# Performance work log

Hardware: AMD Instinct MI355X
Metric: run time of the kernel (lower is better)

## Reference

```python
import jax, jax.numpy as jnp
import numpy as np

B, S, H, A, E = 64, 1024, 1024, 512, 512


def setup_inputs() -> dict:
    key = jax.random.key(0)
    ks = jax.random.split(key, 13)
    sc = 0.02
    return {
        "inputs": jax.random.normal(ks[0], (B, E), jnp.float32),
        "states": jax.random.normal(ks[1], (B, H), jnp.float32),
        "encoded": jax.random.normal(ks[2], (B, S, H), jnp.float32),
        "W_enc": jax.random.normal(ks[3], (H, A), jnp.float32) * sc,
        "b_enc": jax.random.normal(ks[4], (A,), jnp.float32) * sc,
        "W_dec": jax.random.normal(ks[5], (H, A), jnp.float32) * sc,
        "b_dec": jax.random.normal(ks[6], (A,), jnp.float32) * sc,
        "w_out": jax.random.normal(ks[7], (A,), jnp.float32) * sc,
        "b_out": jax.random.normal(ks[8], (1,), jnp.float32) * sc,
        "W_ih": jax.random.normal(ks[9], (E + H, 3 * H), jnp.float32) * sc,
        "b_ih": jax.random.normal(ks[10], (3 * H,), jnp.float32) * sc,
        "W_hh": jax.random.normal(ks[11], (H, 3 * H), jnp.float32) * sc,
        "b_hh": jax.random.normal(ks[12], (3 * H,), jnp.float32) * sc,
    }


def reference(inputs, states, encoded, W_enc, b_enc, W_dec, b_dec, w_out, b_out,
              W_ih, b_ih, W_hh, b_hh):
    # setup_memory: project encoder states once  [B,S,H] @ [H,A] -> [B,S,A]
    enc_proj = jnp.einsum('bsh,ha->bsa', encoded, W_enc) + b_enc
    # Bahdanau additive attention
    dec_proj = states @ W_dec + b_dec                       # [B,A]
    scores = jnp.einsum('bsa,a->bs', jnp.tanh(enc_proj + dec_proj[:, None, :]), w_out) + b_out[0]
    weights = jax.nn.softmax(scores, axis=1)                # [B,S]
    attention = jnp.einsum('bs,bsh->bh', weights, encoded)  # [B,H]
    x = jnp.concatenate([inputs, attention], axis=-1)       # [B,E+H]
    # GRUCell (PyTorch gate order r, z, n)
    gi = x @ W_ih + b_ih                                    # [B,3H]
    gh = states @ W_hh + b_hh                               # [B,3H]
    i_r, i_z, i_n = jnp.split(gi, 3, axis=-1)
    h_r, h_z, h_n = jnp.split(gh, 3, axis=-1)
    r = jax.nn.sigmoid(i_r + h_r)
    z = jax.nn.sigmoid(i_z + h_z)
    n = jnp.tanh(i_n + r * h_n)
    h_new = (1.0 - z) * n + z * states
    return h_new
```

## Files before the change

kernel.cpp:

```cpp
#include <hip/hip_runtime.h>
#include <hip/hip_bf16.h>


typedef __attribute__((ext_vector_type(8))) __bf16 bf16x8;
typedef __attribute__((ext_vector_type(4))) __bf16 bf16x4;
typedef __attribute__((ext_vector_type(4))) float f32x4;

__device__ __forceinline__ float fast_tanh(float x) {
  float xa = fminf(fmaxf(x, -15.f), 15.f);
  float e = __expf(2.f * xa);
  return (e - 1.f) / (e + 1.f);
}

#define GLOAD16(G, L)                                                              \
  __builtin_amdgcn_global_load_lds(                                                \
      (const __attribute__((address_space(1))) unsigned int*)(const void*)(G),     \
      (__attribute__((address_space(3))) unsigned int*)(void*)(L), 16, 0, 0)

__global__ __launch_bounds__(256) void conv_kernel(const float* __restrict__ in,
                                                   __bf16* __restrict__ out, long n16) {
  long stride = (long)gridDim.x * 256;
  for (long i = (long)blockIdx.x * 256 + threadIdx.x; i < n16; i += stride) {
    const f32x4* p = (const f32x4*)(in + i * 16);
    f32x4 v0 = p[0], v1 = p[1], v2 = p[2], v3 = p[3];
    bf16x8 o0, o1;
#pragma unroll
    for (int j = 0; j < 4; ++j) {
      o0[j] = (__bf16)v0[j]; o0[4 + j] = (__bf16)v1[j];
      o1[j] = (__bf16)v2[j]; o1[4 + j] = (__bf16)v3[j];
    }
    *(bf16x8*)(out + i * 16) = o0;
    *(bf16x8*)(out + i * 16 + 8) = o1;
  }
}

__global__ __launch_bounds__(256) void wenc_t_kernel(const float* __restrict__ W,
                                                     __bf16* __restrict__ Wt) {
  __shared__ float tile[32][33];
  int k0 = blockIdx.x * 32, a0 = blockIdx.y * 32;
  int tid = threadIdx.x;
  int r = tid >> 3, c4 = (tid & 7) * 4;
  f32x4 v = *(const f32x4*)(W + (long)(k0 + r) * 512 + a0 + c4);
  tile[r][c4 + 0] = v.x; tile[r][c4 + 1] = v.y;
  tile[r][c4 + 2] = v.z; tile[r][c4 + 3] = v.w;
  __syncthreads();
  int a = tid >> 3, k4 = (tid & 7) * 4;
  bf16x4 o = { (__bf16)tile[k4 + 0][a], (__bf16)tile[k4 + 1][a],
               (__bf16)tile[k4 + 2][a], (__bf16)tile[k4 + 3][a] };
  *(bf16x4*)(Wt + (long)(a0 + a) * 1024 + k0 + k4) = o;
}

__global__ __launch_bounds__(256) void dec_proj_kernel(
    const float* __restrict__ states, const float* __restrict__ W_dec,
    const float* __restrict__ b_enc, const float* __restrict__ b_dec,
    float* __restrict__ addv) {
  int b = blockIdx.x, tid = threadIdx.x;
  int a = blockIdx.y * 256 + tid;
  __shared__ float sl[1024];
  for (int i = tid; i < 1024; i += 256) sl[i] = states[b * 1024 + i];
  __syncthreads();
  float c0 = 0.f, c1 = 0.f, c2 = 0.f, c3 = 0.f;
#pragma unroll 4
  for (int i = 0; i < 256; ++i) {
    c0 += sl[i]         * W_dec[(i)        * 512 + a];
    c1 += sl[i + 256]   * W_dec[(i + 256)  * 512 + a];
    c2 += sl[i + 512]   * W_dec[(i + 512)  * 512 + a];
    c3 += sl[i + 768]   * W_dec[(i + 768)  * 512 + a];
  }
  addv[b * 512 + a] = c0 + c1 + c2 + c3 + b_enc[a] + b_dec[a];
}

__global__ __launch_bounds__(512, 2) void enc_score_kernel(
    const __bf16* __restrict__ encB,
    const __bf16* __restrict__ Wt,
    const float* __restrict__ addv,
    const float* __restrict__ w_out,
    float* __restrict__ psc)
{
  __shared__ __attribute__((aligned(16))) char smem[102400];
  float* red = (float*)(smem + 98304);

  const int d = blockIdx.x;
  const int xcd = d & 7;
  const int slot = d >> 3;
  const int bn = slot & 1;
  const int bm = ((slot >> 1) << 3) | xcd;

  const int tid = threadIdx.x;
  const int lane = tid & 63;
  const int wid = tid >> 6;
  const int wr = wid >> 2;
  const int wc = wid & 3;
  const int lr = lane & 15;
  const int lkb = lane >> 4;

  const long row0 = (long)bm * 256;
  const int col0 = bn * 256;

  const int sk8 = (tid & 3) ^ ((tid >> 3) & 3);
  const __bf16* gA = encB + (row0 + (tid >> 2)) * 1024 + sk8 * 8;
  const __bf16* gB = Wt + (long)(col0 + (tid >> 2)) * 1024 + sk8 * 8;
  const int ldsW = wid * 1024;

  const int foff = (lkb ^ ((lr >> 1) & 3)) << 4;
  const int aRowB = (wr * 128 + lr) * 64;
  const int bColB = (wc * 64 + lr) * 64;

  f32x4 acc[8][4];
#pragma unroll
  for (int m = 0; m < 8; ++m)
#pragma unroll
    for (int n = 0; n < 4; ++n) acc[m][n] = (f32x4){0.f, 0.f, 0.f, 0.f};

#define STAGE(SBUF, KT) do {                                                       \
    const __bf16* _a = gA + (KT) * 32;                                             \
    const __bf16* _b = gB + (KT) * 32;                                             \
    GLOAD16(_a,          smem + (SBUF) * 16384 + ldsW);                            \
    GLOAD16(_a + 131072, smem + (SBUF) * 16384 + 8192 + ldsW);                     \
    GLOAD16(_b,          smem + 49152 + (SBUF) * 16384 + ldsW);                    \
    GLOAD16(_b + 131072, smem + 49152 + (SBUF) * 16384 + 8192 + ldsW);             \
    __builtin_amdgcn_sched_barrier(0);                                             \
  } while (0)

#define COMPUTE(CBUF) do {                                                         \
    const char* _Ab = smem + (CBUF) * 16384;                                       \
    const char* _Bb = smem + 49152 + (CBUF) * 16384;                               \
    bf16x8 _af[8], _bv[4];                                                         \
    _Pragma("unroll") for (int _m = 0; _m < 8; ++_m)                               \
      _af[_m] = *(const bf16x8*)(_Ab + aRowB + _m * 1024 + foff);                  \
    _Pragma("unroll") for (int _n = 0; _n < 4; ++_n)                               \
      _bv[_n] = *(const bf16x8*)(_Bb + bColB + _n * 1024 + foff);                  \
    __builtin_amdgcn_s_setprio(1);                                                 \
    _Pragma("unroll") for (int _m = 0; _m < 8; ++_m)                               \
      _Pragma("unroll") for (int _n = 0; _n < 4; ++_n)                             \
        acc[_m][_n] =                                                              \
            __builtin_amdgcn_mfma_f32_16x16x32_bf16(_af[_m], _bv[_n], acc[_m][_n], 0, 0, 0); \
    __builtin_amdgcn_s_setprio(0);                                                 \
  } while (0)

#define ITER(KT, CBUF, SBUF) do {                                                  \
    asm volatile("s_waitcnt vmcnt(4)" ::: "memory");                               \
    __builtin_amdgcn_sched_barrier(0);                                             \
    __builtin_amdgcn_s_barrier();                                                  \
    __builtin_amdgcn_sched_barrier(0);                                             \
    COMPUTE(CBUF);                                                                 \
    asm volatile("s_waitcnt lgkmcnt(0)" ::: "memory");                             \
    __builtin_amdgcn_sched_barrier(0);                                             \
    __builtin_amdgcn_s_barrier();                                                  \
    __builtin_amdgcn_sched_barrier(0);                                             \
    STAGE(SBUF, (KT) + 2);                                                         \
  } while (0)

  STAGE(0, 0);
  STAGE(1, 1);

  for (int k3 = 0; k3 < 30; k3 += 3) {
    ITER(k3 + 0, 0, 2);
    ITER(k3 + 1, 1, 0);
    ITER(k3 + 2, 2, 1);
  }
  asm volatile("s_waitcnt vmcnt(4)" ::: "memory");
  __builtin_amdgcn_sched_barrier(0);
  __builtin_amdgcn_s_barrier();
  __builtin_amdgcn_sched_barrier(0);
  COMPUTE(0);
  asm volatile("s_waitcnt vmcnt(0)" ::: "memory");
  __builtin_amdgcn_sched_barrier(0);
  __builtin_amdgcn_s_barrier();
  __builtin_amdgcn_sched_barrier(0);
  COMPUTE(1);

#undef STAGE
#undef COMPUTE
#undef ITER

  const int b = bm >> 2;
  const float* addvb = addv + b * 512;
  float rowsum[8][4];
#pragma unroll
  for (int m = 0; m < 8; ++m)
#pragma unroll
    for (int reg = 0; reg < 4; ++reg) rowsum[m][reg] = 0.f;

#pragma unroll
  for (int m = 0; m < 8; ++m) {
#pragma unroll
    for (int n = 0; n < 4; ++n) {
      int col = col0 + wc * 64 + n * 16 + lr;
      float av = addvb[col];
      float wo = w_out[col];
#pragma unroll
      for (int reg = 0; reg < 4; ++reg)
        rowsum[m][reg] += fast_tanh(acc[m][n][reg] + av) * wo;
    }
  }
#pragma unroll
  for (int m = 0; m < 8; ++m)
#pragma unroll
    for (int reg = 0; reg < 4; ++reg) {
      float v = rowsum[m][reg];
      v += __shfl_xor(v, 1, 64);
      v += __shfl_xor(v, 2, 64);
      v += __shfl_xor(v, 4, 64);
      v += __shfl_xor(v, 8, 64);
      rowsum[m][reg] = v;
    }
  __syncthreads();
  if (lr == 0) {
#pragma unroll
    for (int m = 0; m < 8; ++m)
#pragma unroll
      for (int reg = 0; reg < 4; ++reg)
        red[(wr * 128 + m * 16 + lkb * 4 + reg) * 4 + wc] = rowsum[m][reg];
  }
  __syncthreads();
  if (tid < 256)
    psc[(long)bn * 65536 + row0 + tid] =
        red[tid * 4] + red[tid * 4 + 1] + red[tid * 4 + 2] + red[tid * 4 + 3];
}

__global__ __launch_bounds__(256) void softmax_kernel(const float* __restrict__ psc,
                                                      float* __restrict__ wts) {
  int b = blockIdx.x, tid = threadIdx.x;
  __shared__ float sred[8];
  float sc[4];
  float mx = -1e30f;
#pragma unroll
  for (int i = 0; i < 4; ++i) {
    long r = (long)b * 1024 + tid + i * 256;
    sc[i] = psc[r] + psc[65536 + r];
    mx = fmaxf(mx, sc[i]);
  }
  for (int off = 1; off < 64; off <<= 1) mx = fmaxf(mx, __shfl_xor(mx, off, 64));
  if ((tid & 63) == 0) sred[tid >> 6] = mx;
  __syncthreads();
  mx = fmaxf(fmaxf(sred[0], sred[1]), fmaxf(sred[2], sred[3]));
  float e[4], sum = 0.f;
#pragma unroll
  for (int i = 0; i < 4; ++i) {
    e[i] = __expf(sc[i] - mx);
    sum += e[i];
  }
  for (int off = 1; off < 64; off <<= 1) sum += __shfl_xor(sum, off, 64);
  if ((tid & 63) == 0) sred[4 + (tid >> 6)] = sum;
  __syncthreads();
  sum = sred[4] + sred[5] + sred[6] + sred[7];
  float inv = 1.f / sum;
#pragma unroll
  for (int i = 0; i < 4; ++i) wts[(long)b * 1024 + tid + i * 256] = e[i] * inv;
}

__global__ __launch_bounds__(128) void att_part_bf16_kernel(const __bf16* __restrict__ encB,
                                                            const float* __restrict__ wts,
                                                            float* __restrict__ attp) {
  int chunk = blockIdx.x;
  int b = blockIdx.y;
  int tid = threadIdx.x;
  const __bf16* base = encB + ((long)b * 1024 + chunk * 64) * 1024 + tid * 8;
  const float* w = wts + b * 1024 + chunk * 64;
  float a0[8], a1[8];
#pragma unroll
  for (int j = 0; j < 8; ++j) { a0[j] = 0.f; a1[j] = 0.f; }
#pragma unroll 4
  for (int s = 0; s < 64; s += 2) {
    bf16x8 v0 = *(const bf16x8*)(base + (long)s * 1024);
    bf16x8 v1 = *(const bf16x8*)(base + (long)(s + 1) * 1024);
    float w0 = w[s], w1 = w[s + 1];
#pragma unroll
    for (int j = 0; j < 8; ++j) {
      a0[j] += (float)v0[j] * w0;
      a1[j] += (float)v1[j] * w1;
    }
  }
  float* o = attp + ((long)(b * 16 + chunk)) * 1024 + tid * 8;
#pragma unroll
  for (int j = 0; j < 8; ++j) o[j] = a0[j] + a1[j];
}

__global__ __launch_bounds__(256) void xcat_kernel(const float* __restrict__ inputs,
                                                   const float* __restrict__ attp,
                                                   float* __restrict__ xcat) {
  int b = blockIdx.y;
  int k = blockIdx.x * 256 + threadIdx.x;
  float v;
  if (k < 512) {
    v = inputs[b * 512 + k];
  } else {
    int h = k - 512;
    v = 0.f;
#pragma unroll
    for (int c = 0; c < 16; ++c) v += attp[((long)(b * 16 + c)) * 1024 + h];
  }
  xcat[(long)b * 1536 + k] = v;
}

__global__ __launch_bounds__(512) void gru_gemv_kernel(
    const float* __restrict__ xcat, const float* __restrict__ states,
    const float* __restrict__ W_ih, const float* __restrict__ b_ih,
    const float* __restrict__ W_hh, const float* __restrict__ b_hh,
    float* __restrict__ gi, float* __restrict__ gh) {
  __shared__ float sx[12288];
  const int dd = blockIdx.x;
  const int xcd = dd & 7;
  const int n = dd >> 3;
  const int cgrp = xcd + 8 * (n >> 3);
  const int bg = n & 7;
  const int tid = threadIdx.x;
  const int lcol = tid & 255;
  const int bsel = (tid >> 8) * 4;

  if (cgrp < 12) {
    const int col = cgrp * 256 + lcol;
    const float* xb = xcat + (long)bg * 8 * 1536;
    for (int i = tid; i < 3072; i += 512) ((f32x4*)sx)[i] = ((const f32x4*)xb)[i];
    __syncthreads();
    float a0 = b_ih[col], a1 = a0, a2 = a0, a3 = a0;
    const float* x0 = sx + (bsel + 0) * 1536;
    const float* x1 = sx + (bsel + 1) * 1536;
    const float* x2 = sx + (bsel + 2) * 1536;
    const float* x3 = sx + (bsel + 3) * 1536;
    for (int k = 0; k < 1536; k += 4) {
      f32x4 v0 = *(const f32x4*)(x0 + k);
      f32x4 v1 = *(const f32x4*)(x1 + k);
      f32x4 v2 = *(const f32x4*)(x2 + k);
      f32x4 v3 = *(const f32x4*)(x3 + k);
#pragma unroll
      for (int j = 0; j < 4; ++j) {
        float w = W_ih[(long)(k + j) * 3072 + col];
        a0 += v0[j] * w; a1 += v1[j] * w; a2 += v2[j] * w; a3 += v3[j] * w;
      }
    }
    long o = (long)(bg * 8 + bsel) * 3072 + col;
    gi[o] = a0; gi[o + 3072] = a1; gi[o + 6144] = a2; gi[o + 9216] = a3;
  } else {
    const int col = (cgrp - 12) * 256 + lcol;
    const float* sb = states + (long)bg * 8 * 1024;
    for (int i = tid; i < 2048; i += 512) ((f32x4*)sx)[i] = ((const f32x4*)sb)[i];
    __syncthreads();
    float a0 = b_hh[col], a1 = a0, a2 = a0, a3 = a0;
    const float* x0 = sx + (bsel + 0) * 1024;
    const float* x1 = sx + (bsel + 1) * 1024;
    const float* x2 = sx + (bsel + 2) * 1024;
    const float* x3 = sx + (bsel + 3) * 1024;
    for (int k = 0; k < 1024; k += 4) {
      f32x4 v0 = *(const f32x4*)(x0 + k);
      f32x4 v1 = *(const f32x4*)(x1 + k);
      f32x4 v2 = *(const f32x4*)(x2 + k);
      f32x4 v3 = *(const f32x4*)(x3 + k);
#pragma unroll
      for (int j = 0; j < 4; ++j) {
        float w = W_hh[(long)(k + j) * 3072 + col];
        a0 += v0[j] * w; a1 += v1[j] * w; a2 += v2[j] * w; a3 += v3[j] * w;
      }
    }
    long o = (long)(bg * 8 + bsel) * 3072 + col;
    gh[o] = a0; gh[o + 3072] = a1; gh[o + 6144] = a2; gh[o + 9216] = a3;
  }
}

__global__ __launch_bounds__(256) void gate_kernel(const float* __restrict__ gi,
                                                   const float* __restrict__ gh,
                                                   const float* __restrict__ states,
                                                   float* __restrict__ out) {
  int b = blockIdx.y;
  int j = blockIdx.x * 256 + threadIdx.x;
  long o = (long)b * 3072;
  float ir = gi[o + j], hr = gh[o + j];
  float iz = gi[o + 1024 + j], hz = gh[o + 1024 + j];
  float in_ = gi[o + 2048 + j], hn = gh[o + 2048 + j];
  float r = 1.f / (1.f + __expf(-(ir + hr)));
  float z = 1.f / (1.f + __expf(-(iz + hz)));
  float n = fast_tanh(in_ + r * hn);
  out[(long)b * 1024 + j] = (1.f - z) * n + z * states[(long)b * 1024 + j];
}

extern "C" void kernel_launch(void* const* d_in, const int* in_sizes, int n_in,
                              void* d_out, int out_size, void* d_ws, size_t ws_size,
                              hipStream_t stream) {
  const float* inputs  = (const float*)d_in[0];
  const float* states  = (const float*)d_in[1];
  const float* encoded = (const float*)d_in[2];
  const float* W_enc   = (const float*)d_in[3];
  const float* b_enc   = (const float*)d_in[4];
  const float* W_dec   = (const float*)d_in[5];
  const float* b_dec   = (const float*)d_in[6];
  const float* w_out   = (const float*)d_in[7];
  const float* W_ih    = (const float*)d_in[9];
  const float* b_ih    = (const float*)d_in[10];
  const float* W_hh    = (const float*)d_in[11];
  const float* b_hh    = (const float*)d_in[12];
  float* out = (float*)d_out;
  float* ws = (float*)d_ws;

  const long ENC_ELEMS = 64L * 1024 * 1024;
  const long ENCB_FLOATS = ENC_ELEMS / 2;

  __bf16* encB = (__bf16*)ws;
  float* base = ws + ENCB_FLOATS;

  float* addv = base;
  float* psc  = base + 32768;
  float* wts  = base + 163840;
  float* attp = base + 229376;
  float* xcat = base + 1277952;
  float* gi   = base + 1376256;
  float* gh   = base + 1572864;
  __bf16* Wt  = (__bf16*)(base + 1769472);

  conv_kernel<<<4096, 256, 0, stream>>>(encoded, encB, ENC_ELEMS / 16);

  wenc_t_kernel<<<dim3(32, 16), 256, 0, stream>>>(W_enc, Wt);

  dim3 gA(64, 2);
  dec_proj_kernel<<<gA, 256, 0, stream>>>(states, W_dec, b_enc, b_dec, addv);

  enc_score_kernel<<<512, 512, 0, stream>>>(encB, Wt, addv, w_out, psc);

  softmax_kernel<<<64, 256, 0, stream>>>(psc, wts);

  dim3 gD(16, 64);
  att_part_bf16_kernel<<<gD, 128, 0, stream>>>(encB, wts, attp);

  dim3 gE(6, 64);
  xcat_kernel<<<gE, 256, 0, stream>>>(inputs, attp, xcat);

  gru_gemv_kernel<<<192, 512, 0, stream>>>(xcat, states, W_ih, b_ih, W_hh, b_hh, gi, gh);

  dim3 gG(4, 64);
  gate_kernel<<<gG, 256, 0, stream>>>(gi, gh, states, out);
}
```

Measured before the change: 341.4 us.

## Deepen enc-score GEMM pipeline to four LDS stages with one barrier per tile

The bf16 MFMA GEMM in the encoder-score kernel now uses four interleaved A/B LDS buffers instead of three, keeping three k-tiles of global-to-LDS loads in flight. Each iteration waits on the vmcnt counter, hits a single barrier, issues the next stage into the buffer freed by the previous tile, then computes. This replaces the old two-barrier-per-tile scheme. It aims to hide more global load latency and cut synchronisation overhead, at the cost of about 132 KB of shared memory per block.

```diff
diff --git a/kernel.cpp b/kernel.cpp
--- a/kernel.cpp
+++ b/kernel.cpp
@@ -77,8 +77,8 @@
     const float* __restrict__ w_out,
     float* __restrict__ psc)
 {
-  __shared__ __attribute__((aligned(16))) char smem[102400];
-  float* red = (float*)(smem + 98304);
+  __shared__ __attribute__((aligned(16))) char smem[135168];
+  float* red = (float*)(smem + 131072);
 
   const int d = blockIdx.x;
   const int xcd = d & 7;
@@ -115,16 +115,16 @@
 #define STAGE(SBUF, KT) do {                                                       \
     const __bf16* _a = gA + (KT) * 32;                                             \
     const __bf16* _b = gB + (KT) * 32;                                             \
-    GLOAD16(_a,          smem + (SBUF) * 16384 + ldsW);                            \
-    GLOAD16(_a + 131072, smem + (SBUF) * 16384 + 8192 + ldsW);                     \
-    GLOAD16(_b,          smem + 49152 + (SBUF) * 16384 + ldsW);                    \
-    GLOAD16(_b + 131072, smem + 49152 + (SBUF) * 16384 + 8192 + ldsW);             \
-    __builtin_amdgcn_sched_barrier(0);                                             \
+    char* _base = smem + (SBUF) * 32768;                                           \
+    GLOAD16(_a,          _base + ldsW);                                            \
+    GLOAD16(_a + 131072, _base + 8192 + ldsW);                                     \
+    GLOAD16(_b,          _base + 16384 + ldsW);                                    \
+    GLOAD16(_b + 131072, _base + 24576 + ldsW);                                    \
   } while (0)
 
-#define COMPUTE(CBUF) do {                                                         \
-    const char* _Ab = smem + (CBUF) * 16384;                                       \
-    const char* _Bb = smem + 49152 + (CBUF) * 16384;                               \
+#define COMPUTE(COFF) do {                                                         \
+    const char* _Ab = smem + (COFF);                                               \
+    const char* _Bb = _Ab + 16384;                                                 \
     bf16x8 _af[8], _bv[4];                                                         \
     _Pragma("unroll") for (int _m = 0; _m < 8; ++_m)                               \
       _af[_m] = *(const bf16x8*)(_Ab + aRowB + _m * 1024 + foff);                  \
@@ -138,41 +138,33 @@
     __builtin_amdgcn_s_setprio(0);                                                 \
   } while (0)
 
-#define ITER(KT, CBUF, SBUF) do {                                                  \
-    asm volatile("s_waitcnt vmcnt(4)" ::: "memory");                               \
+#define WAITBAR(N) do {                                                            \
+    asm volatile("s_waitcnt vmcnt(" #N ")" ::: "memory");                          \
     __builtin_amdgcn_sched_barrier(0);                                             \
     __builtin_amdgcn_s_barrier();                                                  \
     __builtin_amdgcn_sched_barrier(0);                                             \
-    COMPUTE(CBUF);                                                                 \
-    asm volatile("s_waitcnt lgkmcnt(0)" ::: "memory");                             \
-    __builtin_amdgcn_sched_barrier(0);                                             \
-    __builtin_amdgcn_s_barrier();                                                  \
-    __builtin_amdgcn_sched_barrier(0);                                             \
-    STAGE(SBUF, (KT) + 2);                                                         \
   } while (0)
 
   STAGE(0, 0);
   STAGE(1, 1);
-
-  for (int k3 = 0; k3 < 30; k3 += 3) {
-    ITER(k3 + 0, 0, 2);
-    ITER(k3 + 1, 1, 0);
-    ITER(k3 + 2, 2, 1);
-  }
-  asm volatile("s_waitcnt vmcnt(4)" ::: "memory");
-  __builtin_amdgcn_sched_barrier(0);
-  __builtin_amdgcn_s_barrier();
-  __builtin_amdgcn_sched_barrier(0);
-  COMPUTE(0);
-  asm volatile("s_waitcnt vmcnt(0)" ::: "memory");
-  __builtin_amdgcn_sched_barrier(0);
-  __builtin_amdgcn_s_barrier();
-  __builtin_amdgcn_sched_barrier(0);
-  COMPUTE(1);
+  STAGE(2, 2);
+
+  for (int kt = 0; kt < 29; ++kt) {
+    WAITBAR(8);
+    STAGE((kt + 3) & 3, kt + 3);
+    __builtin_amdgcn_sched_barrier(0);
+    COMPUTE((kt & 3) * 32768);
+  }
+  WAITBAR(8);
+  COMPUTE(1 * 32768);
+  WAITBAR(4);
+  COMPUTE(2 * 32768);
+  WAITBAR(0);
+  COMPUTE(3 * 32768);
 
 #undef STAGE
 #undef COMPUTE
-#undef ITER
+#undef WAITBAR
 
   const int b = bm >> 2;
   const float* addvb = addv + b * 512;
```

After: 337.2 us. No clear change (-1.2%).
